# Kernel tuning notes

Measured on AMD Instinct MI355X. Metric: run time of the kernel, lower is better.

The kernel has to match this reference:

```python
import jax, jax.numpy as jnp
import numpy as np
from jax import lax

B, N, CIN, COUT, R, K = 4, 16384, 64, 128, 32, 3
VOX_EPS = 1e-6
BN3D_EPS = 1e-4
BN1D_EPS = 1e-5
LRELU_SLOPE = 0.1


def setup_inputs() -> dict:
    key = jax.random.key(0)
    ks = jax.random.split(key, 20)
    d = {}
    d['features'] = jax.random.normal(ks[0], (B, N, CIN), jnp.float32)
    d['coords'] = jax.random.normal(ks[1], (B, N, 3), jnp.float32)
    # Conv3D #1: (D,H,W,Cin,Cout) + bias
    d['conv1_w'] = jax.random.normal(ks[2], (K, K, K, CIN, COUT), jnp.float32) * 0.02
    d['conv1_b'] = jax.random.normal(ks[3], (COUT,), jnp.float32) * 0.02
    d['bn1_g'] = jax.random.uniform(ks[4], (COUT,), jnp.float32, 0.75, 1.25)
    d['bn1_b'] = jax.random.normal(ks[5], (COUT,), jnp.float32) * 0.1
    d['bn1_m'] = jax.random.normal(ks[6], (COUT,), jnp.float32) * 0.1
    d['bn1_v'] = jax.random.uniform(ks[7], (COUT,), jnp.float32, 0.5, 1.5)
    # Conv3D #2
    d['conv2_w'] = jax.random.normal(ks[8], (K, K, K, COUT, COUT), jnp.float32) * 0.02
    d['conv2_b'] = jax.random.normal(ks[9], (COUT,), jnp.float32) * 0.02
    d['bn2_g'] = jax.random.uniform(ks[10], (COUT,), jnp.float32, 0.75, 1.25)
    d['bn2_b'] = jax.random.normal(ks[11], (COUT,), jnp.float32) * 0.1
    d['bn2_m'] = jax.random.normal(ks[12], (COUT,), jnp.float32) * 0.1
    d['bn2_v'] = jax.random.uniform(ks[13], (COUT,), jnp.float32, 0.5, 1.5)
    # Point SharedMLP: Conv1D k=1 -> matmul, + BN + ReLU
    d['pw'] = jax.random.normal(ks[14], (CIN, COUT), jnp.float32) * 0.05
    d['pb'] = jax.random.normal(ks[15], (COUT,), jnp.float32) * 0.02
    d['pbn_g'] = jax.random.uniform(ks[16], (COUT,), jnp.float32, 0.75, 1.25)
    d['pbn_b'] = jax.random.normal(ks[17], (COUT,), jnp.float32) * 0.1
    d['pbn_m'] = jax.random.normal(ks[18], (COUT,), jnp.float32) * 0.1
    d['pbn_v'] = jax.random.uniform(ks[19], (COUT,), jnp.float32, 0.5, 1.5)
    return d


def _bn(x, g, b, m, v, eps):
    return (x - m) * (g * lax.rsqrt(v + eps)) + b


def _leaky_relu(x):
    return jnp.where(x >= 0, x, LRELU_SLOPE * x)


def _pvconv(features, coords, conv1_w, conv1_b, bn1_g, bn1_b, bn1_m, bn1_v,
            conv2_w, conv2_b, bn2_g, bn2_b, bn2_m, bn2_v,
            pw, pb, pbn_g, pbn_b, pbn_m, pbn_v):
    r = R
    # ---- Voxelization (normalize coords, scatter-average into grid) ----
    c = lax.stop_gradient(coords)                                   # (B,N,3)
    nc = c - jnp.mean(c, axis=1, keepdims=True)
    denom = jnp.max(jnp.linalg.norm(nc, axis=2, keepdims=True), axis=1, keepdims=True) * 2.0 + VOX_EPS
    nc = nc / denom + 0.5
    nc = jnp.clip(nc * r, 0.0, r - 1)                                # (B,N,3) in [0, r-1]
    vox = jnp.round(nc).astype(jnp.int32)                            # (B,N,3)

    batch_off = jnp.arange(B, dtype=jnp.int32)[:, None] * (r * r * r)
    lin = batch_off + vox[..., 0] * (r * r) + vox[..., 1] * r + vox[..., 2]  # (B,N)
    lin = lin.reshape(-1)
    feat_flat = features.reshape(-1, CIN)
    sums = jax.ops.segment_sum(feat_flat, lin, num_segments=B * r * r * r)   # (B*r^3,Cin)
    cnts = jax.ops.segment_sum(jnp.ones((B * N,), jnp.float32), lin, num_segments=B * r * r * r)
    cnts = jnp.where(cnts == 0, 1.0, cnts)
    grid = (sums / cnts[:, None]).reshape(B, r, r, r, CIN)           # (B,r,r,r,Cin)

    # ---- Voxel branch: Conv3D -> BN -> LeakyReLU (x2) ----
    dn = ('NDHWC', 'DHWIO', 'NDHWC')
    g = lax.conv_general_dilated(grid, conv1_w, (1, 1, 1), 'SAME', dimension_numbers=dn) + conv1_b
    g = _leaky_relu(_bn(g, bn1_g, bn1_b, bn1_m, bn1_v, BN3D_EPS))
    g = lax.conv_general_dilated(g, conv2_w, (1, 1, 1), 'SAME', dimension_numbers=dn) + conv2_b
    g = _leaky_relu(_bn(g, bn2_g, bn2_b, bn2_m, bn2_v, BN3D_EPS))    # (B,r,r,r,Cout)

    # ---- Trilinear devoxelize: gather 8 corners with interpolation weights ----
    g_flat = g.reshape(B, r * r * r, COUT)
    c0 = jnp.floor(nc).astype(jnp.int32)                             # (B,N,3)
    frac = nc - c0.astype(nc.dtype)
    c1 = jnp.minimum(c0 + 1, r - 1)
    vox_pts = jnp.zeros((B, N, COUT), jnp.float32)
    for dx in (0, 1):
        for dy in (0, 1):
            for dz in (0, 1):
                ix = c1[..., 0] if dx else c0[..., 0]
                iy = c1[..., 1] if dy else c0[..., 1]
                iz = c1[..., 2] if dz else c0[..., 2]
                w = ((frac[..., 0] if dx else 1.0 - frac[..., 0]) *
                     (frac[..., 1] if dy else 1.0 - frac[..., 1]) *
                     (frac[..., 2] if dz else 1.0 - frac[..., 2]))   # (B,N)
                idx = ix * (r * r) + iy * r + iz                      # (B,N)
                gathered = jnp.take_along_axis(g_flat, idx[..., None], axis=1)  # (B,N,Cout)
                vox_pts = vox_pts + w[..., None] * gathered

    # ---- Point branch: SharedMLP (1x1 conv -> BN -> ReLU) ----
    pf = jnp.einsum('bnc,cd->bnd', features, pw) + pb
    pf = jax.nn.relu(_bn(pf, pbn_g, pbn_b, pbn_m, pbn_v, BN1D_EPS))

    return vox_pts + pf                                              # (B,N,Cout)


def reference(features, coords, conv1_w, conv1_b, bn1_g, bn1_b, bn1_m, bn1_v,
              conv2_w, conv2_b, bn2_g, bn2_b, bn2_m, bn2_v,
              pw, pb, pbn_g, pbn_b, pbn_m, pbn_v):
    fused = _pvconv(features, coords, conv1_w, conv1_b, bn1_g, bn1_b, bn1_m, bn1_v,
                    conv2_w, conv2_b, bn2_g, bn2_b, bn2_m, bn2_v,
                    pw, pb, pbn_g, pbn_b, pbn_m, pbn_v)
    return (fused, coords)
```

## Files before the change

### kernel.cpp

```cpp
#include <hip/hip_runtime.h>
#include <hip/hip_bf16.h>

constexpr int B    = 4;
constexpr int N    = 16384;
constexpr int CIN  = 64;
constexpr int COUT = 128;
constexpr int R    = 32;
constexpr int R3   = R * R * R;
constexpr int RP   = 34;
constexpr int RP3  = RP * RP * RP;
constexpr float VOX_EPS   = 1e-6f;
constexpr float BN3D_EPS  = 1e-4f;
constexpr float BN1D_EPS  = 1e-5f;
constexpr float LRELU     = 0.1f;

typedef __attribute__((ext_vector_type(8))) short bf16x8;
typedef __attribute__((ext_vector_type(4))) float f32x4;
typedef __attribute__((ext_vector_type(8))) unsigned short u16x8;

__device__ inline float bf2f(ushort u) {
    union { unsigned int i; float f; } x; x.i = ((unsigned int)u) << 16; return x.f;
}
__device__ inline ushort f2bf(float f) {
    union { float f; unsigned int i; } x; x.f = f;
    unsigned int r = x.i + 0x7fffu + ((x.i >> 16) & 1u);
    return (ushort)(r >> 16);
}

__device__ inline int swz(int base, int z) {
    return (base ^ (z & 3) ^ ((z >> 2) & 3)) & 3;
}

__global__ __launch_bounds__(256) void k_stats_sum(const float* __restrict__ coords,
                                                   float* __restrict__ stats) {
    int blk = blockIdx.x;
    int b = blk >> 4, stripe = blk & 15;
    const float* c = coords + ((size_t)b * N + stripe * 1024) * 3;
    float sx = 0.f, sy = 0.f, sz = 0.f;
    for (int i = threadIdx.x; i < 1024; i += 256) {
        sx += c[i * 3 + 0];
        sy += c[i * 3 + 1];
        sz += c[i * 3 + 2];
    }
    __shared__ float red[256];
    float vals[3] = {sx, sy, sz};
    for (int k = 0; k < 3; ++k) {
        red[threadIdx.x] = vals[k];
        __syncthreads();
        for (int s = 128; s > 0; s >>= 1) {
            if (threadIdx.x < s) red[threadIdx.x] += red[threadIdx.x + s];
            __syncthreads();
        }
        if (threadIdx.x == 0) atomicAdd(&stats[b * 8 + k], red[0]);
        __syncthreads();
    }
}

__global__ __launch_bounds__(256) void k_stats_max(const float* __restrict__ coords,
                                                   float* __restrict__ stats) {
    int blk = blockIdx.x;
    int b = blk >> 4, stripe = blk & 15;
    const float invN = 1.0f / (float)N;
    float mx = stats[b * 8 + 0] * invN;
    float my = stats[b * 8 + 1] * invN;
    float mz = stats[b * 8 + 2] * invN;
    const float* c = coords + ((size_t)b * N + stripe * 1024) * 3;
    float mm = 0.f;
    for (int i = threadIdx.x; i < 1024; i += 256) {
        float dx = c[i * 3 + 0] - mx;
        float dy = c[i * 3 + 1] - my;
        float dz = c[i * 3 + 2] - mz;
        mm = fmaxf(mm, sqrtf(dx * dx + dy * dy + dz * dz));
    }
    __shared__ float red[256];
    red[threadIdx.x] = mm;
    __syncthreads();
    for (int s = 128; s > 0; s >>= 1) {
        if (threadIdx.x < s) red[threadIdx.x] = fmaxf(red[threadIdx.x], red[threadIdx.x + s]);
        __syncthreads();
    }
    if (threadIdx.x == 0)
        atomicMax((unsigned*)&stats[b * 8 + 3], __float_as_uint(red[0]));
}

__device__ inline void compute_nc(const float* __restrict__ coords,
                                  const float* __restrict__ stats,
                                  int p, int b, float& nx, float& ny, float& nz) {
    const float invN = 1.0f / (float)N;
    float mmax = __uint_as_float(((const unsigned*)stats)[b * 8 + 3]);
    float denom = mmax * 2.0f + VOX_EPS;
    float cx = coords[(size_t)p * 3 + 0];
    float cy = coords[(size_t)p * 3 + 1];
    float cz = coords[(size_t)p * 3 + 2];
    nx = (cx - stats[b * 8 + 0] * invN) / denom + 0.5f;
    ny = (cy - stats[b * 8 + 1] * invN) / denom + 0.5f;
    nz = (cz - stats[b * 8 + 2] * invN) / denom + 0.5f;
    nx = fminf(fmaxf(nx * (float)R, 0.f), (float)(R - 1));
    ny = fminf(fmaxf(ny * (float)R, 0.f), (float)(R - 1));
    nz = fminf(fmaxf(nz * (float)R, 0.f), (float)(R - 1));
}

__global__ __launch_bounds__(256) void k_scatter(const float* __restrict__ coords,
                                                 const float* __restrict__ feats,
                                                 const float* __restrict__ stats,
                                                 float* __restrict__ sums,
                                                 float* __restrict__ cnt) {
    int sub = threadIdx.x >> 6;
    int ci  = threadIdx.x & 63;
    int p   = blockIdx.x * 4 + sub;
    __shared__ int s_lin[4];
    if (ci == 0) {
        int b = p >> 14;
        float nx, ny, nz;
        compute_nc(coords, stats, p, b, nx, ny, nz);
        int vx = (int)rintf(nx);
        int vy = (int)rintf(ny);
        int vz = (int)rintf(nz);
        int lin = ((b * R + vx) * R + vy) * R + vz;
        s_lin[sub] = lin;
        atomicAdd(&cnt[lin], 1.0f);
    }
    __syncthreads();
    atomicAdd(&sums[(size_t)s_lin[sub] * CIN + ci], feats[(size_t)p * CIN + ci]);
}

__global__ __launch_bounds__(256) void k_zero_border(ushort* __restrict__ buf, int nchunks) {
    int i = blockIdx.x * 256 + threadIdx.x;
    if (i >= nchunks) return;
    int v = i >> 2;
    int r = v % RP3;
    int z = r % RP;
    int t = r / RP;
    int y = t % RP;
    int x = (t / RP) % RP;
    if (x == 0 || x == RP - 1 || y == 0 || y == RP - 1 || z == 0 || z == RP - 1)
        *(uint4*)(buf + (size_t)i * 8) = make_uint4(0u, 0u, 0u, 0u);
}

__global__ __launch_bounds__(256) void k_finalize(const float* __restrict__ sums,
                                                  const float* __restrict__ cnt,
                                                  ushort* __restrict__ gridp) {
    int i = blockIdx.x * 256 + threadIdx.x;
    float c = cnt[i >> 6];
    float val = sums[i] / (c == 0.f ? 1.f : c);
    int ci = i & 63;
    int v = i >> 6;
    int vz = v & 31, vy = (v >> 5) & 31, vx = (v >> 10) & 31, b = v >> 15;
    size_t o = ((((size_t)(b * 2 + (ci >> 5)) * RP + vx + 1) * RP + vy + 1) * RP + vz + 1) * 32
               + (ci & 31);
    gridp[o] = f2bf(val);
}

__global__ __launch_bounds__(256) void k_wq_all(const float* __restrict__ w1,
                                                const float* __restrict__ w2,
                                                const float* __restrict__ pw,
                                                ushort* __restrict__ wq) {
    int idx = blockIdx.x * 256 + threadIdx.x;
    int g = idx >> 12;
    const float* src; int gl;
    if (g < 54)       { src = w1; gl = g; }
    else if (g < 162) { src = w2; gl = g - 54; }
    else              { src = pw; gl = g - 162; }
    int j    = idx & 7;
    int lane = (idx >> 3) & 63;
    int nt   = (idx >> 9) & 7;
    int k = gl * 32 + ((lane >> 4) << 3) + j;
    int n = nt * 16 + (lane & 15);
    wq[idx] = f2bf(src[(size_t)k * COUT + n]);
}

template <int CI, bool PLANAR_OUT>
__global__ __launch_bounds__(256, 3) void k_conv_mfma(const ushort* __restrict__ in,
                                                      const ushort* __restrict__ wq,
                                                      const float* __restrict__ bias,
                                                      const float* __restrict__ bng,
                                                      const float* __restrict__ bnb,
                                                      const float* __restrict__ bnm,
                                                      const float* __restrict__ bnv,
                                                      ushort* __restrict__ out) {
    constexpr int NCHI = CI / 32;
    __shared__ __align__(16) ushort sl[18 * RP * 32];

    int bid = blockIdx.x;
    int Y = bid & 7;
    int x = (bid >> 3) & 31;
    int b = bid >> 8;
    int y0 = Y * 4;
    int tid = threadIdx.x;
    int wave = tid >> 6, lane = tid & 63, quad = lane >> 4, l16 = lane & 15;
    int wm = wave >> 1, wn = wave & 1;

    f32x4 acc[4][4] = {};

    for (int cc = 0; cc < NCHI; ++cc) {
        const ushort* base = in + (((size_t)(b * NCHI + cc) * RP + x) * RP + y0) * RP * 32;
        __syncthreads();
        for (int t = tid; t < 18 * 136; t += 256) {
            int row = t / 136;
            int r   = t - row * 136;
            int X = row / 6, Yl = row - X * 6;
            uint4 v = *(const uint4*)(base + ((size_t)(X * RP + Yl) * RP) * 32 + r * 8);
            int z = r >> 2, ch = r & 3;
            *(uint4*)(sl + ((row * RP + z) * 4 + swz(ch, z)) * 8) = v;
        }
        __syncthreads();

        for (int tap = 0; tap < 27; ++tap) {
            int dx = tap / 9, rem = tap - dx * 9;
            int dy = rem / 3, dz = rem - dy * 3;

            const ushort* bp = wq + ((size_t)((tap * NCHI + cc) * 8 + wn * 4) * 64 + lane) * 8;
            bf16x8 bfr[4], afr[4];
#pragma unroll
            for (int nt = 0; nt < 4; ++nt)
                bfr[nt] = *(const bf16x8*)(bp + nt * 512);
#pragma unroll
            for (int mt = 0; mt < 4; ++mt) {
                int row18 = dx * 6 + wm * 2 + (mt >> 1) + dy;
                int zrow = ((mt & 1) << 4) + l16 + dz;
                afr[mt] = *(const bf16x8*)(sl + ((row18 * RP + zrow) * 4 + swz(quad, zrow)) * 8);
            }
#pragma unroll
            for (int mt = 0; mt < 4; ++mt)
#pragma unroll
                for (int nt = 0; nt < 4; ++nt)
                    acc[mt][nt] = __builtin_amdgcn_mfma_f32_16x16x32_bf16(
                        afr[mt], bfr[nt], acc[mt][nt], 0, 0, 0);
        }
    }

    float sc[4], sb[4], bs[4];
#pragma unroll
    for (int nt = 0; nt < 4; ++nt) {
        int co = wn * 64 + nt * 16 + l16;
        sc[nt] = bng[co] * rsqrtf(bnv[co] + BN3D_EPS);
        sb[nt] = bnb[co] - bnm[co] * sc[nt];
        bs[nt] = bias[co];
    }
#pragma unroll
    for (int mt = 0; mt < 4; ++mt) {
#pragma unroll
        for (int reg = 0; reg < 4; ++reg) {
            int m = wm * 64 + mt * 16 + quad * 4 + reg;
            int i = m >> 5, z = m & 31;
#pragma unroll
            for (int nt = 0; nt < 4; ++nt) {
                float v = (acc[mt][nt][reg] + bs[nt]) * sc[nt] + sb[nt];
                v = v >= 0.f ? v : LRELU * v;
                int co = wn * 64 + nt * 16 + l16;
                if (PLANAR_OUT) {
                    size_t o = ((((size_t)(b * 4 + (co >> 5)) * RP + (x + 1)) * RP
                                 + (y0 + i + 1)) * RP + (z + 1)) * 32 + (co & 31);
                    out[o] = f2bf(v);
                } else {
                    size_t o = (((size_t)(b * R + x) * R + (y0 + i)) * R + z) * COUT + co;
                    out[o] = f2bf(v);
                }
            }
        }
    }
}

__global__ __launch_bounds__(256, 2) void k_devox(const float* __restrict__ coords,
                                                  const float* __restrict__ feats,
                                                  const float* __restrict__ stats,
                                                  const ushort* __restrict__ g2,
                                                  const ushort* __restrict__ pwq,
                                                  const float* __restrict__ pb,
                                                  const float* __restrict__ pg,
                                                  const float* __restrict__ pbb,
                                                  const float* __restrict__ pm,
                                                  const float* __restrict__ pv,
                                                  float* __restrict__ out) {
    __shared__ __align__(16) ushort sfeat[128 * 64];
    __shared__ __align__(16) ushort smlp[128 * 128];
    __shared__ int   sidx[128 * 8];
    __shared__ float swt[128 * 8];

    int blk = blockIdx.x, tid = threadIdx.x;
    int wave = tid >> 6, lane = tid & 63, quad = lane >> 4, l16 = lane & 15;
    int p0 = blk * 128;

    if (tid < 128) {
        int p = p0 + tid, b = p >> 14;
        float nx, ny, nz;
        compute_nc(coords, stats, p, b, nx, ny, nz);
        int cx0 = (int)floorf(nx), cy0 = (int)floorf(ny), cz0 = (int)floorf(nz);
        float fx = nx - (float)cx0, fy = ny - (float)cy0, fz = nz - (float)cz0;
        int cx1 = min(cx0 + 1, R - 1), cy1 = min(cy0 + 1, R - 1), cz1 = min(cz0 + 1, R - 1);
#pragma unroll
        for (int k = 0; k < 8; ++k) {
            int dx = (k >> 2) & 1, dy = (k >> 1) & 1, dz = k & 1;
            int ix = dx ? cx1 : cx0;
            int iy = dy ? cy1 : cy0;
            int iz = dz ? cz1 : cz0;
            sidx[tid * 8 + k] = (((b * R + ix) * R + iy) * R + iz) * COUT;
            swt[tid * 8 + k] = (dx ? fx : 1.f - fx) * (dy ? fy : 1.f - fy) * (dz ? fz : 1.f - fz);
        }
    }
    for (int i = 0; i < 4; ++i) {
        int c = i * 256 + tid;
        int p = c >> 3, ch = c & 7;
        const float* src = feats + (size_t)(p0 + p) * CIN + ch * 8;
        float4 f0 = *(const float4*)src;
        float4 f1 = *(const float4*)(src + 4);
        u16x8 u;
        u[0] = f2bf(f0.x); u[1] = f2bf(f0.y); u[2] = f2bf(f0.z); u[3] = f2bf(f0.w);
        u[4] = f2bf(f1.x); u[5] = f2bf(f1.y); u[6] = f2bf(f1.z); u[7] = f2bf(f1.w);
        *(u16x8*)&sfeat[(p * 8 + (ch ^ (p & 7))) * 8] = u;
    }
    __syncthreads();

    f32x4 acc[8][2] = {};
#pragma unroll
    for (int cc = 0; cc < 2; ++cc) {
        const ushort* bp = pwq + ((size_t)(cc * 8 + wave * 2) * 64 + lane) * 8;
        bf16x8 b0 = *(const bf16x8*)bp;
        bf16x8 b1 = *(const bf16x8*)(bp + 512);
#pragma unroll
        for (int mt = 0; mt < 8; ++mt) {
            int prow = mt * 16 + l16;
            int ch = cc * 4 + quad;
            bf16x8 a = *(const bf16x8*)&sfeat[(prow * 8 + (ch ^ (prow & 7))) * 8];
            acc[mt][0] = __builtin_amdgcn_mfma_f32_16x16x32_bf16(a, b0, acc[mt][0], 0, 0, 0);
            acc[mt][1] = __builtin_amdgcn_mfma_f32_16x16x32_bf16(a, b1, acc[mt][1], 0, 0, 0);
        }
    }

    int co0 = wave * 32 + l16, co1 = co0 + 16;
    {
        float sc0 = pg[co0] * rsqrtf(pv[co0] + BN1D_EPS);
        float sb0 = pbb[co0] - pm[co0] * sc0;
        float bs0 = pb[co0];
        float sc1 = pg[co1] * rsqrtf(pv[co1] + BN1D_EPS);
        float sb1 = pbb[co1] - pm[co1] * sc1;
        float bs1 = pb[co1];
#pragma unroll
        for (int mt = 0; mt < 8; ++mt) {
#pragma unroll
            for (int reg = 0; reg < 4; ++reg) {
                int pl = mt * 16 + quad * 4 + reg;
                smlp[pl * 128 + co0] = f2bf(fmaxf((acc[mt][0][reg] + bs0) * sc0 + sb0, 0.f));
                smlp[pl * 128 + co1] = f2bf(fmaxf((acc[mt][1][reg] + bs1) * sc1 + sb1, 0.f));
            }
        }
    }
    __syncthreads();

#pragma unroll
    for (int it = 0; it < 8; ++it) {
        int t = it * 256 + tid;
        int p = t >> 4, c = t & 15;
        float a[8];
        const ushort* m = &smlp[p * 128 + c * 8];
#pragma unroll
        for (int j = 0; j < 8; ++j) a[j] = bf2f(m[j]);
#pragma unroll
        for (int k = 0; k < 8; ++k) {
            int idx = sidx[p * 8 + k];
            float w = swt[p * 8 + k];
            bf16x8 row = *(const bf16x8*)(g2 + (size_t)idx + c * 8);
#pragma unroll
            for (int j = 0; j < 8; ++j) a[j] += w * bf2f(((u16x8)row)[j]);
        }
        float* o = out + (size_t)(p0 + p) * COUT + c * 8;
        *(float4*)o       = make_float4(a[0], a[1], a[2], a[3]);
        *(float4*)(o + 4) = make_float4(a[4], a[5], a[6], a[7]);
    }
}

extern "C" void kernel_launch(void* const* d_in, const int* in_sizes, int n_in,
                              void* d_out, int out_size, void* d_ws, size_t ws_size,
                              hipStream_t stream) {
    const float* feats   = (const float*)d_in[0];
    const float* coords  = (const float*)d_in[1];
    const float* conv1_w = (const float*)d_in[2];
    const float* conv1_b = (const float*)d_in[3];
    const float* bn1_g   = (const float*)d_in[4];
    const float* bn1_b   = (const float*)d_in[5];
    const float* bn1_m   = (const float*)d_in[6];
    const float* bn1_v   = (const float*)d_in[7];
    const float* conv2_w = (const float*)d_in[8];
    const float* conv2_b = (const float*)d_in[9];
    const float* bn2_g   = (const float*)d_in[10];
    const float* bn2_b   = (const float*)d_in[11];
    const float* bn2_m   = (const float*)d_in[12];
    const float* bn2_v   = (const float*)d_in[13];
    const float* pw      = (const float*)d_in[14];
    const float* pb      = (const float*)d_in[15];
    const float* pbn_g   = (const float*)d_in[16];
    const float* pbn_b   = (const float*)d_in[17];
    const float* pbn_m   = (const float*)d_in[18];
    const float* pbn_v   = (const float*)d_in[19];

    char* p = (char*)d_ws;
    float* stats = (float*)p;                        p += 256;
    float* sums  = (float*)p;                        p += (size_t)B * R3 * CIN * 4;
    float* cnt   = (float*)p;                        p += (size_t)B * R3 * 4;
    ushort* gridp = (ushort*)p;                      p += (size_t)B * 2 * RP3 * 32 * 2;
    ushort* g1p   = (ushort*)p;                      p += (size_t)B * 4 * RP3 * 32 * 2;
    ushort* g2b   = (ushort*)p;                      p += (size_t)B * R3 * COUT * 2;
    ushort* wq    = (ushort*)p;                      p += (size_t)164 * 4096 * 2;
    ushort* wq1 = wq;
    ushort* wq2 = wq + 54 * 4096;
    ushort* pwq = wq + 162 * 4096;
    float*  outf  = (float*)d_out;

    hipMemsetAsync(stats, 0, 256 + ((size_t)B * R3 * CIN + (size_t)B * R3) * sizeof(float),
                   stream);
    {
        int nc = B * 6 * RP3 * 4;
        k_zero_border<<<(nc + 255) / 256, 256, 0, stream>>>(gridp, nc);
    }

    k_stats_sum<<<64, 256, 0, stream>>>(coords, stats);
    k_stats_max<<<64, 256, 0, stream>>>(coords, stats);
    k_scatter<<<(B * N) / 4, 256, 0, stream>>>(coords, feats, stats, sums, cnt);
    k_finalize<<<(B * R3 * CIN) / 256, 256, 0, stream>>>(sums, cnt, gridp);

    k_wq_all<<<(164 * 4096) / 256, 256, 0, stream>>>(conv1_w, conv2_w, pw, wq);

    k_conv_mfma<CIN, true><<<B * R * (R / 4), 256, 0, stream>>>(
        gridp, wq1, conv1_b, bn1_g, bn1_b, bn1_m, bn1_v, g1p);
    k_conv_mfma<COUT, false><<<B * R * (R / 4), 256, 0, stream>>>(
        g1p, wq2, conv2_b, bn2_g, bn2_b, bn2_m, bn2_v, g2b);

    k_devox<<<(B * N) / 128, 256, 0, stream>>>(coords, feats, stats, g2b, pwq, pb,
                                               pbn_g, pbn_b, pbn_m, pbn_v, outf);

    hipMemcpyAsync(outf + (size_t)B * N * COUT, coords, (size_t)B * N * 3 * sizeof(float),
                   hipMemcpyDeviceToDevice, stream);
}
```

Baseline: 347.1 us.

## Replace atomic scatter-average voxelization with counting sort and per-voxel gather

Voxelization no longer does 64 float atomics per point into a large fp32 sum grid. It now counts points per voxel with integer atomics, builds per-voxel offsets with a two-level prefix scan, fills a sorted point-index list, and has each voxel gather and average its points' features directly into the padded bf16 grid. This removes the big sums memset and the contended float atomics, at the cost of three extra small kernel launches. The gather step does irregular, serialized reads for voxels that hold many points.

```diff
diff --git a/kernel.cpp b/kernel.cpp
--- a/kernel.cpp
+++ b/kernel.cpp
@@ -9,6 +9,7 @@
 constexpr int R3   = R * R * R;
 constexpr int RP   = 34;
 constexpr int RP3  = RP * RP * RP;
+constexpr int NVOX = B * R3;
 constexpr float VOX_EPS   = 1e-6f;
 constexpr float BN3D_EPS  = 1e-4f;
 constexpr float BN1D_EPS  = 1e-5f;
@@ -100,28 +101,83 @@
     nz = fminf(fmaxf(nz * (float)R, 0.f), (float)(R - 1));
 }
 
-__global__ __launch_bounds__(256) void k_scatter(const float* __restrict__ coords,
-                                                 const float* __restrict__ feats,
-                                                 const float* __restrict__ stats,
-                                                 float* __restrict__ sums,
-                                                 float* __restrict__ cnt) {
-    int sub = threadIdx.x >> 6;
-    int ci  = threadIdx.x & 63;
-    int p   = blockIdx.x * 4 + sub;
-    __shared__ int s_lin[4];
-    if (ci == 0) {
-        int b = p >> 14;
-        float nx, ny, nz;
-        compute_nc(coords, stats, p, b, nx, ny, nz);
-        int vx = (int)rintf(nx);
-        int vy = (int)rintf(ny);
-        int vz = (int)rintf(nz);
-        int lin = ((b * R + vx) * R + vy) * R + vz;
-        s_lin[sub] = lin;
-        atomicAdd(&cnt[lin], 1.0f);
-    }
+__global__ __launch_bounds__(256) void k_count(const float* __restrict__ coords,
+                                               const float* __restrict__ stats,
+                                               int* __restrict__ cnt,
+                                               int* __restrict__ plin,
+                                               int* __restrict__ pslot) {
+    int p = blockIdx.x * 256 + threadIdx.x;
+    int b = p >> 14;
+    float nx, ny, nz;
+    compute_nc(coords, stats, p, b, nx, ny, nz);
+    int lin = ((b * R + (int)rintf(nx)) * R + (int)rintf(ny)) * R + (int)rintf(nz);
+    plin[p] = lin;
+    pslot[p] = atomicAdd(&cnt[lin], 1);
+}
+
+__global__ __launch_bounds__(256) void k_scan1(const int* __restrict__ cnt,
+                                               int* __restrict__ base,
+                                               int* __restrict__ btot) {
+    __shared__ int s[256];
+    int g = blockIdx.x * 256 + threadIdx.x;
+    int val = cnt[g];
+    s[threadIdx.x] = val;
     __syncthreads();
-    atomicAdd(&sums[(size_t)s_lin[sub] * CIN + ci], feats[(size_t)p * CIN + ci]);
+    for (int off = 1; off < 256; off <<= 1) {
+        int v = threadIdx.x >= off ? s[threadIdx.x - off] : 0;
+        __syncthreads();
+        s[threadIdx.x] += v;
+        __syncthreads();
+    }
+    base[g] = s[threadIdx.x] - val;
+    if (threadIdx.x == 255) btot[blockIdx.x] = s[255];
+}
+
+__global__ __launch_bounds__(512) void k_scan2(const int* __restrict__ btot,
+                                               int* __restrict__ boff) {
+    __shared__ int s[512];
+    int val = btot[threadIdx.x];
+    s[threadIdx.x] = val;
+    __syncthreads();
+    for (int off = 1; off < 512; off <<= 1) {
+        int v = threadIdx.x >= off ? s[threadIdx.x - off] : 0;
+        __syncthreads();
+        s[threadIdx.x] += v;
+        __syncthreads();
+    }
+    boff[threadIdx.x] = s[threadIdx.x] - val;
+}
+
+__global__ __launch_bounds__(256) void k_fill(const int* __restrict__ plin,
+                                              const int* __restrict__ pslot,
+                                              const int* __restrict__ base,
+                                              const int* __restrict__ boff,
+                                              int* __restrict__ order) {
+    int p = blockIdx.x * 256 + threadIdx.x;
+    int lin = plin[p];
+    order[base[lin] + boff[lin >> 8] + pslot[p]] = p;
+}
+
+__global__ __launch_bounds__(256) void k_gather(const float* __restrict__ feats,
+                                                const int* __restrict__ cnt,
+                                                const int* __restrict__ base,
+                                                const int* __restrict__ boff,
+                                                const int* __restrict__ order,
+                                                ushort* __restrict__ gridp) {
+    int v = blockIdx.x * 4 + (threadIdx.x >> 6);
+    int lane = threadIdx.x & 63;
+    int c = cnt[v];
+    int bs = base[v] + boff[v >> 8];
+    float acc = 0.f;
+    for (int j = 0; j < c; ++j) {
+        int p = order[bs + j];
+        acc += feats[(size_t)p * CIN + lane];
+    }
+    float val = acc / (float)(c == 0 ? 1 : c);
+    int vz = v & 31, vy = (v >> 5) & 31, vx = (v >> 10) & 31, b = v >> 15;
+    size_t o = ((((size_t)(b * 2 + (lane >> 5)) * RP + vx + 1) * RP + vy + 1) * RP + (vz + 1)) * 32
+               + (lane & 31);
+    gridp[o] = f2bf(val);
 }
 
 __global__ __launch_bounds__(256) void k_zero_border(ushort* __restrict__ buf, int nchunks) {
@@ -135,20 +191,6 @@
     int x = (t / RP) % RP;
     if (x == 0 || x == RP - 1 || y == 0 || y == RP - 1 || z == 0 || z == RP - 1)
         *(uint4*)(buf + (size_t)i * 8) = make_uint4(0u, 0u, 0u, 0u);
-}
-
-__global__ __launch_bounds__(256) void k_finalize(const float* __restrict__ sums,
-                                                  const float* __restrict__ cnt,
-                                                  ushort* __restrict__ gridp) {
-    int i = blockIdx.x * 256 + threadIdx.x;
-    float c = cnt[i >> 6];
-    float val = sums[i] / (c == 0.f ? 1.f : c);
-    int ci = i & 63;
-    int v = i >> 6;
-    int vz = v & 31, vy = (v >> 5) & 31, vx = (v >> 10) & 31, b = v >> 15;
-    size_t o = ((((size_t)(b * 2 + (ci >> 5)) * RP + vx + 1) * RP + vy + 1) * RP + vz + 1) * 32
-               + (ci & 31);
-    gridp[o] = f2bf(val);
 }
 
 __global__ __launch_bounds__(256) void k_wq_all(const float* __restrict__ w1,
@@ -395,8 +437,13 @@
 
     char* p = (char*)d_ws;
     float* stats = (float*)p;                        p += 256;
-    float* sums  = (float*)p;                        p += (size_t)B * R3 * CIN * 4;
-    float* cnt   = (float*)p;                        p += (size_t)B * R3 * 4;
+    int*   cnt   = (int*)p;                          p += (size_t)NVOX * 4;
+    int*   plin  = (int*)p;                          p += (size_t)B * N * 4;
+    int*   pslot = (int*)p;                          p += (size_t)B * N * 4;
+    int*   base  = (int*)p;                          p += (size_t)NVOX * 4;
+    int*   btot  = (int*)p;                          p += 512 * 4;
+    int*   boff  = (int*)p;                          p += 512 * 4;
+    int*   order = (int*)p;                          p += (size_t)B * N * 4;
     ushort* gridp = (ushort*)p;                      p += (size_t)B * 2 * RP3 * 32 * 2;
     ushort* g1p   = (ushort*)p;                      p += (size_t)B * 4 * RP3 * 32 * 2;
     ushort* g2b   = (ushort*)p;                      p += (size_t)B * R3 * COUT * 2;
@@ -406,8 +453,7 @@
     ushort* pwq = wq + 162 * 4096;
     float*  outf  = (float*)d_out;
 
-    hipMemsetAsync(stats, 0, 256 + ((size_t)B * R3 * CIN + (size_t)B * R3) * sizeof(float),
-                   stream);
+    hipMemsetAsync(stats, 0, 256 + (size_t)NVOX * 4, stream);
     {
         int nc = B * 6 * RP3 * 4;
         k_zero_border<<<(nc + 255) / 256, 256, 0, stream>>>(gridp, nc);
@@ -415,8 +461,12 @@
 
     k_stats_sum<<<64, 256, 0, stream>>>(coords, stats);
     k_stats_max<<<64, 256, 0, stream>>>(coords, stats);
-    k_scatter<<<(B * N) / 4, 256, 0, stream>>>(coords, feats, stats, sums, cnt);
-    k_finalize<<<(B * R3 * CIN) / 256, 256, 0, stream>>>(sums, cnt, gridp);
+
+    k_count<<<(B * N) / 256, 256, 0, stream>>>(coords, stats, cnt, plin, pslot);
+    k_scan1<<<NVOX / 256, 256, 0, stream>>>(cnt, base, btot);
+    k_scan2<<<1, 512, 0, stream>>>(btot, boff);
+    k_fill<<<(B * N) / 256, 256, 0, stream>>>(plin, pslot, base, boff, order);
+    k_gather<<<NVOX / 4, 256, 0, stream>>>(feats, cnt, base, boff, order, gridp);
 
     k_wq_all<<<(164 * 4096) / 256, 256, 0, stream>>>(conv1_w, conv2_w, pw, wq);
 
```

Result: slower. 354.1 us (+2.0%).
